# Optimization experiments

Measured on AMD Instinct MI355X. Metric: run time of the kernel, lower is better.

Reference implementation:

```python
import jax, jax.numpy as jnp
import numpy as np
import math

D_MODEL, NHEAD, N_LAYERS = 128, 8, 4
LAYER_NAMES = ("self", "cross", "self", "cross")
B, H, W = 2, 128, 160
MID = D_MODEL
D_FF = 2 * D_MODEL
BN_EPS = 1e-5
LN_EPS = 1e-5
ATTN_EPS = 1e-6


def setup_inputs() -> dict:
    key = jax.random.key(0)
    ks = iter(jax.random.split(key, 64))

    def rn(shape, scale):
        return jax.random.normal(next(ks), shape, dtype=jnp.float32) * scale

    inp = {}
    inp["ref_feature"] = rn((B, D_MODEL, H, W), 1.0)
    inp["src_feature"] = rn((B, D_MODEL, H, W), 1.0)
    K = np.array([[200.0, 0.0, W / 2.0], [0.0, 200.0, H / 2.0], [0.0, 0.0, 1.0]], np.float32)

    def make_proj(tx):
        E = np.eye(4, dtype=np.float32); E[0, 3] = tx
        P = np.eye(4, dtype=np.float32); P[:3, :4] = K @ E[:3, :4]
        return np.broadcast_to(P, (B, 4, 4)).astype(np.float32).copy()

    rp, sp = make_proj(0.0), make_proj(10.0)
    inp["ref_proj"] = jnp.asarray(rp)
    inp["src_proj"] = jnp.asarray(sp)
    inp["ref_img2world"] = jnp.asarray(np.linalg.inv(rp))
    inp["src_img2world"] = jnp.asarray(np.linalg.inv(sp))
    inp["depth_hypo"] = 500.0 + 100.0 * jax.random.uniform(next(ks), (B, 1, H, W), dtype=jnp.float32)
    xav = 0.08  # ~xavier std for 128x128
    inp["attn_w"] = rn((N_LAYERS, 4, D_MODEL, D_MODEL), xav)  # q,k,v,out
    inp["attn_b"] = jnp.zeros((N_LAYERS, 4, D_MODEL), jnp.float32)
    inp["ffn_w1"] = rn((N_LAYERS, D_MODEL, D_FF), 0.07)
    inp["ffn_b1"] = jnp.zeros((N_LAYERS, D_FF), jnp.float32)
    inp["ffn_w2"] = rn((N_LAYERS, D_FF, D_MODEL), 0.07)
    inp["ffn_b2"] = jnp.zeros((N_LAYERS, D_MODEL), jnp.float32)
    inp["ln_g"] = jnp.ones((N_LAYERS, 2, D_MODEL), jnp.float32)
    inp["ln_b"] = jnp.zeros((N_LAYERS, 2, D_MODEL), jnp.float32)
    inp["rc_w"] = rn((MID, 1, 3, 3), 0.01)
    inp["rc_b"] = jnp.zeros((MID,), jnp.float32)
    inp["bn2_g"] = jnp.ones((MID,), jnp.float32)
    inp["bn2_b"] = jnp.zeros((MID,), jnp.float32)
    inp["cc_w"] = rn((MID, D_MODEL), xav)
    inp["cc_b"] = jnp.zeros((D_MODEL,), jnp.float32)
    inp["bn1_g"] = jnp.ones((16,), jnp.float32)
    inp["bn1_b"] = jnp.zeros((16,), jnp.float32)
    inp["fc1_w"] = rn((16, MID), 0.16)
    inp["fc1_b"] = jnp.zeros((MID,), jnp.float32)
    inp["fc2_w"] = rn((MID, MID), xav)
    inp["fc2_b"] = jnp.zeros((MID,), jnp.float32)
    inp["ser_w"] = rn((MID, MID), xav)
    inp["ser_b"] = jnp.zeros((MID,), jnp.float32)
    inp["see_w"] = rn((MID, MID), xav)
    inp["see_b"] = jnp.zeros((MID,), jnp.float32)
    return inp


def sine_pe(d_model, Hh, Ww):
    # PositionEncodingSine (temp_bug_fix=True), computed only on the [H,W] slice
    y_pos = jnp.arange(1, Hh + 1, dtype=jnp.float32)[:, None] * jnp.ones((1, Ww), jnp.float32)
    x_pos = jnp.ones((Hh, 1), jnp.float32) * jnp.arange(1, Ww + 1, dtype=jnp.float32)[None, :]
    div = jnp.exp(jnp.arange(0, d_model // 2, 2, dtype=jnp.float32) * (-math.log(10000.0) / (d_model // 2)))[:, None, None]
    pe = jnp.stack([jnp.sin(x_pos * div), jnp.cos(x_pos * div), jnp.sin(y_pos * div), jnp.cos(y_pos * div)], axis=1)
    return pe.reshape(d_model, Hh, Ww)


def grid_sample_bilinear(feat, grid):
    # feat [B,C,Hs,Ws], grid [B,P,2] normalized to [-1,1]; align_corners=True, zeros padding
    Bn, C, Hs, Ws = feat.shape
    P = grid.shape[1]
    x = (grid[..., 0] + 1.0) * 0.5 * (Ws - 1)
    y = (grid[..., 1] + 1.0) * 0.5 * (Hs - 1)
    x0, y0 = jnp.floor(x), jnp.floor(y)
    wx, wy = x - x0, y - y0
    flat = feat.reshape(Bn, C, Hs * Ws)

    def gather(xi, yi):
        valid = (xi >= 0) & (xi <= Ws - 1) & (yi >= 0) & (yi <= Hs - 1)
        xi_c = jnp.clip(xi, 0, Ws - 1).astype(jnp.int32)
        yi_c = jnp.clip(yi, 0, Hs - 1).astype(jnp.int32)
        idx = yi_c * Ws + xi_c  # [B,P]
        v = jnp.take_along_axis(flat, jnp.broadcast_to(idx[:, None, :], (Bn, C, P)), axis=2)
        return v * valid[:, None, :].astype(feat.dtype)

    v00 = gather(x0, y0)
    v01 = gather(x0 + 1, y0)
    v10 = gather(x0, y0 + 1)
    v11 = gather(x0 + 1, y0 + 1)
    wx, wy = wx[:, None, :], wy[:, None, :]
    return v00 * (1 - wx) * (1 - wy) + v01 * wx * (1 - wy) + v10 * (1 - wx) * wy + v11 * wx * wy


def homo_warp_ref_to_src(feat, ref_proj, src_proj, depth):
    # homo_warping_pe with fea='ref': proj = ref_proj @ inv(src_proj)
    Bn, C, Hs, Ws = feat.shape
    _, D, Hr, Wr = depth.shape
    proj = jnp.einsum('bij,bjk->bik', ref_proj, jnp.linalg.inv(src_proj))
    rot, trans = proj[:, :3, :3], proj[:, :3, 3]
    yy, xx = jnp.meshgrid(jnp.arange(Hr, dtype=jnp.float32), jnp.arange(Wr, dtype=jnp.float32), indexing='ij')
    xyz = jnp.stack([xx.ravel(), yy.ravel(), jnp.ones(Hr * Wr, jnp.float32)], 0)  # [3, P]
    rot_xyz = jnp.einsum('bij,jp->bip', rot, xyz)  # [B,3,P]
    pxyz = rot_xyz[:, :, None, :] * depth.reshape(Bn, 1, D, Hr * Wr) + trans[:, :, None, None]
    z = pxyz[:, 2]
    z = jnp.where(z == 0, 1e-9, z)
    gx = (pxyz[:, 0] / z) / ((Ws - 1) / 2.0) - 1.0
    gy = (pxyz[:, 1] / z) / ((Hs - 1) / 2.0) - 1.0
    grid = jax.lax.stop_gradient(jnp.stack([gx, gy], -1).reshape(Bn, D * Hr * Wr, 2))  # torch no_grad
    out = grid_sample_bilinear(feat, grid)
    return out.reshape(Bn, C, D, Hr, Wr)


def layer_norm(x, g, b):
    mu = x.mean(-1, keepdims=True)
    var = ((x - mu) ** 2).mean(-1, keepdims=True)
    return (x - mu) * jax.lax.rsqrt(var + LN_EPS) * g + b


def encoder_layer(x, src, w, bb, w1, b1f, w2, b2f, g, bt):
    N, L, d = x.shape
    h, dh = NHEAD, d // NHEAD
    q = (x @ w[0] + bb[0]).reshape(N, L, h, dh)
    k = (src @ w[1] + bb[1]).reshape(N, -1, h, dh)
    v = (src @ w[2] + bb[2]).reshape(N, -1, h, dh)
    Q = jax.nn.elu(q) + 1.0
    K = jax.nn.elu(k) + 1.0
    KV = jnp.einsum('nshd,nshm->nhmd', K, v)
    Z = 1.0 / (jnp.einsum('nlhd,nhd->nlh', Q, K.sum(1)) + ATTN_EPS)
    V = jnp.einsum('nlhd,nhmd,nlh->nlhm', Q, KV, Z).reshape(N, L, d)
    x = x + (V @ w[3] + bb[3])
    x = layer_norm(x, g[0], bt[0])
    y = jax.nn.relu(x @ w1 + b1f) @ w2 + b2f
    return layer_norm(x + y, g[1], bt[1])


def cam_encode(feat, cam16, rc_w, rc_b, bn2_g, bn2_b, cc_w, cc_b, bn1_g, bn1_b,
               fc1_w, fc1_b, fc2_w, fc2_b, ser_w, ser_b, see_w, see_b):
    inv_std = 1.0 / jnp.sqrt(1.0 + BN_EPS)  # eval-mode BN, running stats (0,1)
    mlp_in = cam16 * inv_std * bn1_g + bn1_b
    hmap = jax.lax.conv_general_dilated(feat, rc_w, (1, 1), 'SAME', dimension_numbers=('NCHW', 'OIHW', 'NCHW')) + rc_b[None, :, None, None]
    hmap = jax.nn.relu(hmap * inv_std * bn2_g[None, :, None, None] + bn2_b[None, :, None, None])
    se = jax.nn.relu(mlp_in @ fc1_w + fc1_b) @ fc2_w + fc2_b  # [B, MID]
    gate = jax.nn.sigmoid(jax.nn.relu(se @ ser_w + ser_b) @ see_w + see_b)
    ctx = hmap * gate[:, :, None, None]
    return jnp.einsum('bchw,co->bohw', ctx, cc_w) + cc_b[None, :, None, None]


def reference(ref_feature, src_feature, ref_img2world, src_img2world, ref_proj, src_proj, depth_hypo,
              attn_w, attn_b, ffn_w1, ffn_b1, ffn_w2, ffn_b2, ln_g, ln_b,
              rc_w, rc_b, bn2_g, bn2_b, cc_w, cc_b, bn1_g, bn1_b,
              fc1_w, fc1_b, fc2_w, fc2_b, ser_w, ser_b, see_w, see_b):
    Bn, C, Hh, Ww = ref_feature.shape
    pe = sine_pe(C, Hh, Ww)[None]
    ref_ctx = cam_encode(depth_hypo, ref_img2world.reshape(Bn, 16), rc_w, rc_b, bn2_g, bn2_b,
                         cc_w, cc_b, bn1_g, bn1_b, fc1_w, fc1_b, fc2_w, fc2_b,
                         ser_w, ser_b, see_w, see_b)
    src_ctx = homo_warp_ref_to_src(ref_ctx, ref_proj, src_proj, depth_hypo)[:, :, 0]
    ref = (ref_feature + pe + ref_ctx).reshape(Bn, C, Hh * Ww).transpose(0, 2, 1)
    src = (src_feature + pe + src_ctx).reshape(Bn, C, Hh * Ww).transpose(0, 2, 1)
    for i, name in enumerate(LAYER_NAMES):
        p = (attn_w[i], attn_b[i], ffn_w1[i], ffn_b1[i], ffn_w2[i], ffn_b2[i], ln_g[i], ln_b[i])
        if name == 'self':
            ref = encoder_layer(ref, ref, *p)
            src = encoder_layer(src, src, *p)
        else:
            ref = encoder_layer(ref, src, *p)
            src = encoder_layer(src, ref, *p)
    return jnp.stack([ref, src])  # [2, B, H*W, C]
```

## Files before the change

kernel.cpp:

```cpp
#include <hip/hip_runtime.h>
#include <math.h>

#define BN 2
#define HH 128
#define WW 160
#define HWn (HH*WW)
#define CD 128
#define TT (BN*HWn)
#define TOKN ((size_t)TT*CD)

typedef __attribute__((ext_vector_type(8))) short bf16x8;
typedef __attribute__((ext_vector_type(4))) float f32x4;
typedef __attribute__((ext_vector_type(4))) unsigned short u16x4;

__device__ __forceinline__ float b2f(unsigned short s){
  unsigned u = ((unsigned)s) << 16;
  return __builtin_bit_cast(float, u);
}
__device__ __forceinline__ unsigned short f2b(float f){
  unsigned u = __builtin_bit_cast(unsigned, f);
  u = (u + 0x7fffu + ((u >> 16) & 1u)) >> 16;
  return (unsigned short)u;
}

__global__ void k_small(const float* __restrict__ ref_proj, const float* __restrict__ src_i2w,
                        const float* __restrict__ cam16,
                        const float* __restrict__ bn1_g, const float* __restrict__ bn1_b,
                        const float* __restrict__ fc1_w, const float* __restrict__ fc1_b,
                        const float* __restrict__ fc2_w, const float* __restrict__ fc2_b,
                        const float* __restrict__ ser_w, const float* __restrict__ ser_b,
                        const float* __restrict__ see_w, const float* __restrict__ see_b,
                        float* __restrict__ projsmall, float* __restrict__ gate){
  __shared__ float mi[BN][16], t1[BN][128], t2[BN][128];
  int tid = threadIdx.x;
  const float inv_std = rsqrtf(1.0f + 1e-5f);
  if (tid < 32){
    int b = tid >> 4, idx = tid & 15, i = idx >> 2, k = idx & 3;
    float acc = 0.f;
    for (int j = 0; j < 4; j++) acc += ref_proj[b*16 + i*4 + j] * src_i2w[b*16 + j*4 + k];
    if (i < 3 && k < 3) projsmall[b*12 + i*3 + k] = acc;
    if (i < 3 && k == 3) projsmall[b*12 + 9 + i] = acc;
    mi[b][idx] = cam16[b*16 + idx] * inv_std * bn1_g[idx] + bn1_b[idx];
  }
  __syncthreads();
  int b = tid >> 7, c = tid & 127;
  float a = 0.f;
  for (int j = 0; j < 16; j++) a += mi[b][j] * fc1_w[j*128 + c];
  t1[b][c] = fmaxf(a + fc1_b[c], 0.f);
  __syncthreads();
  a = 0.f;
  for (int k = 0; k < 128; k++) a += t1[b][k] * fc2_w[k*128 + c];
  t2[b][c] = a + fc2_b[c];
  __syncthreads();
  a = 0.f;
  for (int k = 0; k < 128; k++) a += t2[b][k] * ser_w[k*128 + c];
  t1[b][c] = fmaxf(a + ser_b[c], 0.f);
  __syncthreads();
  a = 0.f;
  for (int k = 0; k < 128; k++) a += t1[b][k] * see_w[k*128 + c];
  a += see_b[c];
  gate[b*128 + c] = 1.f / (1.f + __expf(-a));
}

__global__ __launch_bounds__(256) void k_wconv(const float* __restrict__ attn_w,
      const float* __restrict__ ffn_w1, const float* __restrict__ ffn_w2,
      const float* __restrict__ cc_w, unsigned short* __restrict__ wt){
  int i = blockIdx.x*256 + threadIdx.x;
  float v;
  if (i < 262144){
    int k = i & 127, n = (i >> 7) & 127, lm = i >> 14;
    v = attn_w[((size_t)lm*128 + k)*128 + n];
  } else if (i < 393216){ int j = i - 262144;
    int k = j & 127, n = (j >> 7) & 255, l = j >> 15;
    v = ffn_w1[((size_t)l*128 + k)*256 + n];
  } else if (i < 524288){ int j = i - 393216;
    int k = j & 255, n = (j >> 8) & 127, l = j >> 15;
    v = ffn_w2[((size_t)l*256 + k)*128 + n];
  } else if (i < 540672){ int j = i - 524288;
    int k = j & 127, n = j >> 7;
    v = cc_w[(size_t)k*128 + n];
  } else return;
  wt[i] = f2b(v);
}

__global__ __launch_bounds__(128) void k_hmap(const float* __restrict__ depth,
                       const float* __restrict__ rc_w, const float* __restrict__ rc_b,
                       const float* __restrict__ bn2_g, const float* __restrict__ bn2_b,
                       const float* __restrict__ gate, unsigned short* __restrict__ G){
  int bi = blockIdx.x; int n = bi / HWn; int p = bi - n*HWn;
  int y = p / WW, x = p - y*WW;
  int c = threadIdx.x;
  const float inv_std = rsqrtf(1.f + 1e-5f);
  float acc = 0.f;
#pragma unroll
  for (int ky = 0; ky < 3; ky++){
    int yy = y + ky - 1;
#pragma unroll
    for (int kx = 0; kx < 3; kx++){
      int xx = x + kx - 1;
      float v = (yy >= 0 && yy < HH && xx >= 0 && xx < WW) ? depth[n*HWn + yy*WW + xx] : 0.f;
      acc += v * rc_w[c*9 + ky*3 + kx];
    }
  }
  acc += rc_b[c];
  acc = fmaxf(acc * inv_std * bn2_g[c] + bn2_b[c], 0.f);
  G[(size_t)bi*128 + c] = f2b(acc * gate[n*128 + c]);
}

template<int K, int ACT, int LN>
__global__ __launch_bounds__(256) void k_bgemm6(
    const unsigned short* __restrict__ A, const unsigned short* __restrict__ A2, int ldA,
    const unsigned short* __restrict__ Wt,
    const float* __restrict__ bias, int amask,
    const unsigned short* __restrict__ resid,
    unsigned short* __restrict__ Cbase, size_t secStride, int ldC,
    const float* __restrict__ lng, const float* __restrict__ lnb){
  __shared__ unsigned short Wl[128*128];
  constexpr int NH = K/128;
  int tid = threadIdx.x;
  int wid = tid >> 6, lane = tid & 63;
  int sec = blockIdx.y;
  const unsigned short* Ab = (sec == 0) ? A : A2;
  const unsigned short* Ws = Wt + (size_t)sec*128*K;
  const float* bs = bias + sec*128;
  unsigned short* C = Cbase + (size_t)sec*secStride;
  int r = lane & 15, ks = lane >> 4;
  size_t t0 = (size_t)blockIdx.x*64 + wid*16;
  const unsigned short* ap = Ab + (t0 + r)*ldA + ks*8;
  f32x4 acc[8] = {};
#pragma unroll
  for (int hh = 0; hh < NH; hh++){
    if (hh > 0) __syncthreads();
#pragma unroll
    for (int i = 0; i < 8; i++){
      int idx = i*256 + tid;
      int row = idx >> 4, c8 = idx & 15;
      int c8s = c8 ^ (row & 7);
      *(bf16x8*)&Wl[row*128 + c8s*8] = *(const bf16x8*)(Ws + (size_t)row*K + hh*128 + c8*8);
    }
    __syncthreads();
#pragma unroll
    for (int j = 0; j < 4; j++){
      bf16x8 a = *(const bf16x8*)(ap + hh*128 + j*32);
#pragma unroll
      for (int f = 0; f < 8; f++){
        int row = f*16 + r;
        int c8s = (j*4 + ks) ^ (row & 7);
        bf16x8 w = *(const bf16x8*)&Wl[row*128 + c8s*8];
        acc[f] = __builtin_amdgcn_mfma_f32_16x16x32_bf16(w, a, acc[f], 0, 0, 0);
      }
    }
  }
  bool act = (amask >> sec) & 1;
  size_t trow = t0 + r;
  float vv[8][4];
#pragma unroll
  for (int f = 0; f < 8; f++){
    float4 bi4 = *(const float4*)&bs[f*16 + 4*ks];
    vv[f][0] = acc[f][0] + bi4.x; vv[f][1] = acc[f][1] + bi4.y;
    vv[f][2] = acc[f][2] + bi4.z; vv[f][3] = acc[f][3] + bi4.w;
    if (resid){
      u16x4 rr = *(const u16x4*)(resid + trow*128 + f*16 + 4*ks);
#pragma unroll
      for (int e = 0; e < 4; e++) vv[f][e] += b2f(rr[e]);
    }
    if (act){
#pragma unroll
      for (int e = 0; e < 4; e++){
        float x = vv[f][e];
        if (ACT == 1) x = fmaxf(x, 0.f);
        if (ACT == 2) x = x > 0.f ? x + 1.f : __expf(x);
        vv[f][e] = x;
      }
    }
  }
  if (LN){
    float s = 0.f;
#pragma unroll
    for (int f = 0; f < 8; f++) s += vv[f][0]+vv[f][1]+vv[f][2]+vv[f][3];
    s += __shfl_xor(s, 16, 64); s += __shfl_xor(s, 32, 64);
    float mean = s * (1.f/128.f);
    float q = 0.f;
#pragma unroll
    for (int f = 0; f < 8; f++)
#pragma unroll
      for (int e = 0; e < 4; e++){ float d = vv[f][e]-mean; q += d*d; }
    q += __shfl_xor(q, 16, 64); q += __shfl_xor(q, 32, 64);
    float rstd = rsqrtf(q*(1.f/128.f) + 1e-5f);
#pragma unroll
    for (int f = 0; f < 8; f++){
      float4 g4 = *(const float4*)&lng[f*16 + 4*ks];
      float4 b4 = *(const float4*)&lnb[f*16 + 4*ks];
      vv[f][0] = (vv[f][0]-mean)*rstd*g4.x + b4.x;
      vv[f][1] = (vv[f][1]-mean)*rstd*g4.y + b4.y;
      vv[f][2] = (vv[f][2]-mean)*rstd*g4.z + b4.z;
      vv[f][3] = (vv[f][3]-mean)*rstd*g4.w + b4.w;
    }
  }
#pragma unroll
  for (int f = 0; f < 8; f++){
    u16x4 o;
#pragma unroll
    for (int e = 0; e < 4; e++) o[e] = f2b(vv[f][e]);
    *(u16x4*)(C + trow*ldC + f*16 + 4*ks) = o;
  }
}

__global__ __launch_bounds__(256) void k_fffn(
    const unsigned short* __restrict__ A,
    const unsigned short* __restrict__ W1t, const float* __restrict__ b1,
    const unsigned short* __restrict__ W2t, const float* __restrict__ b2,
    const float* __restrict__ g1, const float* __restrict__ lb1,
    unsigned short* __restrict__ Out){
  __shared__ unsigned short Wl[128*128];
  __shared__ unsigned short Hs[64*256];
  int tid = threadIdx.x;
  int wid = tid >> 6, lane = tid & 63;
  int r = lane & 15, ks = lane >> 4;
  int tl = wid*16 + r;
  size_t trow = (size_t)blockIdx.x*64 + tl;
  const unsigned short* ap = A + trow*128 + ks*8;
  bf16x8 areg[4];
#pragma unroll
  for (int j = 0; j < 4; j++) areg[j] = *(const bf16x8*)(ap + j*32);
  int swl = tl & 7;
#pragma unroll
  for (int hh = 0; hh < 2; hh++){
    if (hh > 0) __syncthreads();
#pragma unroll
    for (int i = 0; i < 8; i++){
      int idx = i*256 + tid;
      int row = idx >> 4, c8 = idx & 15;
      *(bf16x8*)&Wl[row*128 + (c8 ^ (row & 7))*8] =
          *(const bf16x8*)(W1t + (size_t)(hh*128 + row)*128 + c8*8);
    }
    __syncthreads();
    f32x4 acc[8] = {};
#pragma unroll
    for (int j = 0; j < 4; j++){
#pragma unroll
      for (int f = 0; f < 8; f++){
        int row = f*16 + r;
        int c8s = (j*4 + ks) ^ (row & 7);
        bf16x8 w = *(const bf16x8*)&Wl[row*128 + c8s*8];
        acc[f] = __builtin_amdgcn_mfma_f32_16x16x32_bf16(w, areg[j], acc[f], 0, 0, 0);
      }
    }
#pragma unroll
    for (int f = 0; f < 8; f++){
      float4 bi4 = *(const float4*)&b1[hh*128 + f*16 + 4*ks];
      u16x4 o;
      o[0] = f2b(fmaxf(acc[f][0] + bi4.x, 0.f));
      o[1] = f2b(fmaxf(acc[f][1] + bi4.y, 0.f));
      o[2] = f2b(fmaxf(acc[f][2] + bi4.z, 0.f));
      o[3] = f2b(fmaxf(acc[f][3] + bi4.w, 0.f));
      int c8 = hh*16 + 2*f + (ks >> 1);
      *(u16x4*)&Hs[tl*256 + (c8 ^ swl)*8 + 4*(ks & 1)] = o;
    }
  }
  f32x4 acc2[8] = {};
#pragma unroll
  for (int hh = 0; hh < 2; hh++){
    __syncthreads();
#pragma unroll
    for (int i = 0; i < 8; i++){
      int idx = i*256 + tid;
      int row = idx >> 4, c8 = idx & 15;
      *(bf16x8*)&Wl[row*128 + (c8 ^ (row & 7))*8] =
          *(const bf16x8*)(W2t + (size_t)row*256 + hh*128 + c8*8);
    }
    __syncthreads();
#pragma unroll
    for (int j = 0; j < 4; j++){
      bf16x8 a = *(const bf16x8*)&Hs[tl*256 + ((hh*16 + j*4 + ks) ^ swl)*8];
#pragma unroll
      for (int f = 0; f < 8; f++){
        int row = f*16 + r;
        int c8s = (j*4 + ks) ^ (row & 7);
        bf16x8 w = *(const bf16x8*)&Wl[row*128 + c8s*8];
        acc2[f] = __builtin_amdgcn_mfma_f32_16x16x32_bf16(w, a, acc2[f], 0, 0, 0);
      }
    }
  }
  float vv[8][4];
#pragma unroll
  for (int f = 0; f < 8; f++){
    float4 bi4 = *(const float4*)&b2[f*16 + 4*ks];
    u16x4 rr = *(const u16x4*)(A + trow*128 + f*16 + 4*ks);
    vv[f][0] = acc2[f][0] + bi4.x + b2f(rr[0]);
    vv[f][1] = acc2[f][1] + bi4.y + b2f(rr[1]);
    vv[f][2] = acc2[f][2] + bi4.z + b2f(rr[2]);
    vv[f][3] = acc2[f][3] + bi4.w + b2f(rr[3]);
  }
  float s = 0.f;
#pragma unroll
  for (int f = 0; f < 8; f++) s += vv[f][0]+vv[f][1]+vv[f][2]+vv[f][3];
  s += __shfl_xor(s, 16, 64); s += __shfl_xor(s, 32, 64);
  float mean = s * (1.f/128.f);
  float q = 0.f;
#pragma unroll
  for (int f = 0; f < 8; f++)
#pragma unroll
    for (int e = 0; e < 4; e++){ float d = vv[f][e]-mean; q += d*d; }
  q += __shfl_xor(q, 16, 64); q += __shfl_xor(q, 32, 64);
  float rstd = rsqrtf(q*(1.f/128.f) + 1e-5f);
#pragma unroll
  for (int f = 0; f < 8; f++){
    float4 g4 = *(const float4*)&g1[f*16 + 4*ks];
    float4 b4 = *(const float4*)&lb1[f*16 + 4*ks];
    u16x4 o;
    o[0] = f2b((vv[f][0]-mean)*rstd*g4.x + b4.x);
    o[1] = f2b((vv[f][1]-mean)*rstd*g4.y + b4.y);
    o[2] = f2b((vv[f][2]-mean)*rstd*g4.z + b4.z);
    o[3] = f2b((vv[f][3]-mean)*rstd*g4.w + b4.w);
    *(u16x4*)(Out + trow*128 + f*16 + 4*ks) = o;
  }
}

__global__ __launch_bounds__(256) void k_fattn(
    const unsigned short* __restrict__ Q, const unsigned short* __restrict__ X,
    const float* __restrict__ kvfin, const unsigned short* __restrict__ W3,
    const float* __restrict__ b3, const float* __restrict__ g0, const float* __restrict__ b0,
    unsigned short* __restrict__ Out){
  __shared__ unsigned short Wl[128*128];
  __shared__ unsigned short QV[64][136];
  __shared__ float ksums[8][16];
  int tid = threadIdx.x;
  size_t tb = (size_t)blockIdx.x*64;
  int g = (int)(tb / HWn);
  const float* kvb = kvfin + g*2176;
  {
    int row = tid >> 1, half = tid & 1;
    int h = row >> 4, m = row & 15;
    int swz = row & 7;
#pragma unroll
    for (int c8i = 0; c8i < 8; c8i++){
      int c8 = half*8 + c8i;
      bf16x8 val = {};
      if ((c8 >> 1) == h){
        int d0 = (c8 & 1)*8;
        const float* src = kvb + h*272 + m*16 + d0;
#pragma unroll
        for (int e = 0; e < 8; e++) ((unsigned short*)&val)[e] = f2b(src[e]);
      }
      *(bf16x8*)&Wl[row*128 + (c8 ^ swz)*8] = val;
    }
  }
  if (tid < 128) ksums[tid >> 4][tid & 15] = kvb[(tid >> 4)*272 + 256 + (tid & 15)];
  __syncthreads();
  int wid = tid >> 6, lane = tid & 63;
  int r = lane & 15, ks = lane >> 4;
  int tl = wid*16 + r;
  size_t trow = tb + tl;
  f32x4 acc[8] = {};
  float part0 = 0.f, part1 = 0.f, part2 = 0.f, part3 = 0.f;
  int myp = ks >> 1;
  int dlo = (ks & 1)*8;
#pragma unroll
  for (int j = 0; j < 4; j++){
    bf16x8 a = *(const bf16x8*)(Q + trow*128 + j*32 + ks*8);
    float pj = 0.f;
    int hj = 2*j + myp;
#pragma unroll
    for (int e = 0; e < 8; e++)
      pj += b2f(((unsigned short*)&a)[e]) * ksums[hj][dlo + e];
    if (j == 0) part0 = pj; else if (j == 1) part1 = pj;
    else if (j == 2) part2 = pj; else part3 = pj;
#pragma unroll
    for (int f = 0; f < 8; f++){
      int row = f*16 + r;
      int c8s = (j*4 + ks) ^ (row & 7);
      bf16x8 w = *(const bf16x8*)&Wl[row*128 + c8s*8];
      acc[f] = __builtin_amdgcn_mfma_f32_16x16x32_bf16(w, a, acc[f], 0, 0, 0);
    }
  }
  float full0 = part0 + __shfl_xor(part0, 16, 64);
  float full1 = part1 + __shfl_xor(part1, 16, 64);
  float full2 = part2 + __shfl_xor(part2, 16, 64);
  float full3 = part3 + __shfl_xor(part3, 16, 64);
  float oth0 = __shfl_xor(full0, 32, 64);
  float oth1 = __shfl_xor(full1, 32, 64);
  float oth2 = __shfl_xor(full2, 32, 64);
  float oth3 = __shfl_xor(full3, 32, 64);
#pragma unroll
  for (int f = 0; f < 8; f++){
    float fl, ot;
    if (f < 2){ fl = full0; ot = oth0; } else if (f < 4){ fl = full1; ot = oth1; }
    else if (f < 6){ fl = full2; ot = oth2; } else { fl = full3; ot = oth3; }
    float den = ((f & 1) == myp) ? fl : ot;
    float rc = 1.f / (den + 1e-6f);
    u16x4 o;
#pragma unroll
    for (int e = 0; e < 4; e++) o[e] = f2b(acc[f][e] * rc);
    *(u16x4*)&QV[tl][f*16 + 4*ks] = o;
  }
  __syncthreads();
#pragma unroll
  for (int i = 0; i < 8; i++){
    int idx = i*256 + tid;
    int row = idx >> 4, c8 = idx & 15;
    int c8s = c8 ^ (row & 7);
    *(bf16x8*)&Wl[row*128 + c8s*8] = *(const bf16x8*)(W3 + (size_t)row*128 + c8*8);
  }
  __syncthreads();
  f32x4 acc2[8] = {};
#pragma unroll
  for (int j = 0; j < 4; j++){
    bf16x8 a = *(const bf16x8*)&QV[tl][j*32 + ks*8];
#pragma unroll
    for (int f = 0; f < 8; f++){
      int row = f*16 + r;
      int c8s = (j*4 + ks) ^ (row & 7);
      bf16x8 w = *(const bf16x8*)&Wl[row*128 + c8s*8];
      acc2[f] = __builtin_amdgcn_mfma_f32_16x16x32_bf16(w, a, acc2[f], 0, 0, 0);
    }
  }
  float vv[8][4];
#pragma unroll
  for (int f = 0; f < 8; f++){
    float4 bi4 = *(const float4*)&b3[f*16 + 4*ks];
    u16x4 rr = *(const u16x4*)(X + trow*128 + f*16 + 4*ks);
    vv[f][0] = acc2[f][0] + bi4.x + b2f(rr[0]);
    vv[f][1] = acc2[f][1] + bi4.y + b2f(rr[1]);
    vv[f][2] = acc2[f][2] + bi4.z + b2f(rr[2]);
    vv[f][3] = acc2[f][3] + bi4.w + b2f(rr[3]);
  }
  float s = 0.f;
#pragma unroll
  for (int f = 0; f < 8; f++) s += vv[f][0]+vv[f][1]+vv[f][2]+vv[f][3];
  s += __shfl_xor(s, 16, 64); s += __shfl_xor(s, 32, 64);
  float mean = s * (1.f/128.f);
  float q = 0.f;
#pragma unroll
  for (int f = 0; f < 8; f++)
#pragma unroll
    for (int e = 0; e < 4; e++){ float d = vv[f][e]-mean; q += d*d; }
  q += __shfl_xor(q, 16, 64); q += __shfl_xor(q, 32, 64);
  float rstd = rsqrtf(q*(1.f/128.f) + 1e-5f);
#pragma unroll
  for (int f = 0; f < 8; f++){
    float4 g4 = *(const float4*)&g0[f*16 + 4*ks];
    float4 b4 = *(const float4*)&b0[f*16 + 4*ks];
    u16x4 o;
    o[0] = f2b((vv[f][0]-mean)*rstd*g4.x + b4.x);
    o[1] = f2b((vv[f][1]-mean)*rstd*g4.y + b4.y);
    o[2] = f2b((vv[f][2]-mean)*rstd*g4.z + b4.z);
    o[3] = f2b((vv[f][3]-mean)*rstd*g4.w + b4.w);
    *(u16x4*)(Out + trow*128 + f*16 + 4*ks) = o;
  }
}

__global__ __launch_bounds__(256) void k_kvpart(const unsigned short* __restrict__ Kb,
                         const unsigned short* __restrict__ Vb, float* __restrict__ part){
  __shared__ float Ks[16][260], Vs[16][260];
  int bi = blockIdx.x;
  int chunk = bi % 80; int h = (bi / 80) & 7; int g = bi / 640;
  int s0 = chunk * 256;
  int tid = threadIdx.x;
#pragma unroll
  for (int rr = 0; rr < 8; rr++){
    int idx = rr*256 + tid;
    int s = idx >> 3, d2 = idx & 7;
    size_t gg = ((size_t)(g*HWn + s0 + s))*128 + h*16 + d2*2;
    Ks[d2*2  ][s] = b2f(Kb[gg]);
    Ks[d2*2+1][s] = b2f(Kb[gg+1]);
    Vs[d2*2  ][s] = b2f(Vb[gg]);
    Vs[d2*2+1][s] = b2f(Vb[gg+1]);
  }
  __syncthreads();
  int m = tid >> 4, d = tid & 15;
  float acc = 0.f, ksum = 0.f;
#pragma unroll 4
  for (int s4 = 0; s4 < 64; s4++){
    float4 kv = *(const float4*)&Ks[d][s4*4];
    float4 vv = *(const float4*)&Vs[m][s4*4];
    acc  += kv.x*vv.x + kv.y*vv.y + kv.z*vv.z + kv.w*vv.w;
    ksum += kv.x + kv.y + kv.z + kv.w;
  }
  part[(size_t)bi*272 + tid] = acc;
  if (m == 0) part[(size_t)bi*272 + 256 + d] = ksum;
}

__global__ void k_kvreduce(const float* __restrict__ part, float* __restrict__ fin){
  int nh = blockIdx.x;
  int o = threadIdx.x;
  if (o < 272){
    float acc = 0.f;
    for (int c2 = 0; c2 < 80; c2++) acc += part[((size_t)nh*80 + c2)*272 + o];
    fin[nh*272 + o] = acc;
  }
}

__global__ __launch_bounds__(128) void k_warp(const unsigned short* __restrict__ ctxref,
     const float* __restrict__ depth, const float* __restrict__ projs,
     unsigned short* __restrict__ ctxsrc){
  int bi = blockIdx.x; int n = bi / HWn; int p = bi - n*HWn;
  int y = p / WW, x = p - y*WW;
  const float* pr = &projs[n*12];
  float d = depth[n*HWn + p];
  float fx = (float)x, fy = (float)y;
  float px = (pr[0]*fx + pr[1]*fy + pr[2])*d + pr[9];
  float py = (pr[3]*fx + pr[4]*fy + pr[5])*d + pr[10];
  float pz = (pr[6]*fx + pr[7]*fy + pr[8])*d + pr[11];
  if (pz == 0.f) pz = 1e-9f;
  float xs = px/pz, ys = py/pz;
  float x0 = floorf(xs), y0 = floorf(ys);
  float wx = xs - x0, wy = ys - y0;
  int c = threadIdx.x;
  float acc = 0.f;
#pragma unroll
  for (int dy = 0; dy < 2; dy++){
    float cy = y0 + dy;
    float wyv = dy ? wy : 1.f - wy;
#pragma unroll
    for (int dx = 0; dx < 2; dx++){
      float cx = x0 + dx;
      float wxv = dx ? wx : 1.f - wx;
      bool valid = (cx >= 0.f) && (cx <= (float)(WW-1)) && (cy >= 0.f) && (cy <= (float)(HH-1));
      int xi = (int)fminf(fmaxf(cx, 0.f), (float)(WW-1));
      int yi = (int)fminf(fmaxf(cy, 0.f), (float)(HH-1));
      float v = b2f(ctxref[((size_t)(n*HWn) + yi*WW + xi)*128 + c]);
      acc += valid ? wxv*wyv*v : 0.f;
    }
  }
  ctxsrc[(size_t)bi*128 + c] = f2b(acc);
}

__global__ __launch_bounds__(256) void k_build(const float* __restrict__ feat,
      const unsigned short* __restrict__ ctx, unsigned short* __restrict__ out){
  __shared__ float tile[32][33];
  int tx = threadIdx.x, ty = threadIdx.y;
  int p0 = blockIdx.x*32, c0 = blockIdx.y*32, b = blockIdx.z;
  for (int i = ty; i < 32; i += 8)
    tile[i][tx] = feat[((size_t)(b*CD + c0 + i))*HWn + p0 + tx];
  __syncthreads();
  const float LOG1E4_32 = 0.28782313662425572f;
  for (int r = ty; r < 32; r += 8){
    int p = p0 + r, c = c0 + tx;
    int y = p / WW, x = p - y*WW;
    int i = c >> 2, j = c & 3;
    float dv = __expf(-(float)i * LOG1E4_32);
    float pos = (j < 2) ? (float)(x + 1) : (float)(y + 1);
    float arg = pos * dv;
    float pe = (j & 1) ? cosf(arg) : sinf(arg);
    size_t o = ((size_t)(b*HWn) + p)*128 + c;
    out[o] = f2b(tile[tx][r] + pe + b2f(ctx[o]));
  }
}

__global__ __launch_bounds__(256) void k_tofp32(const unsigned short* __restrict__ s,
                                                float* __restrict__ out){
  size_t i = ((size_t)blockIdx.x*256 + threadIdx.x)*4;
  u16x4 v = *(const u16x4*)(s + i);
  float4 o = { b2f(v[0]), b2f(v[1]), b2f(v[2]), b2f(v[3]) };
  *(float4*)(out + i) = o;
}

extern "C" void kernel_launch(void* const* d_in, const int* in_sizes, int n_in,
                              void* d_out, int out_size, void* d_ws, size_t ws_size,
                              hipStream_t stream) {
  const float* ref_feature = (const float*)d_in[0];
  const float* src_feature = (const float*)d_in[1];
  const float* ref_proj    = (const float*)d_in[2];
  const float* ref_i2w     = (const float*)d_in[4];
  const float* src_i2w     = (const float*)d_in[5];
  const float* depth       = (const float*)d_in[6];
  const float* attn_w      = (const float*)d_in[7];
  const float* attn_b      = (const float*)d_in[8];
  const float* ffn_w1      = (const float*)d_in[9];
  const float* ffn_b1      = (const float*)d_in[10];
  const float* ffn_w2      = (const float*)d_in[11];
  const float* ffn_b2      = (const float*)d_in[12];
  const float* ln_g        = (const float*)d_in[13];
  const float* ln_b        = (const float*)d_in[14];
  const float* rc_w        = (const float*)d_in[15];
  const float* rc_b        = (const float*)d_in[16];
  const float* bn2_g       = (const float*)d_in[17];
  const float* bn2_b       = (const float*)d_in[18];
  const float* cc_w        = (const float*)d_in[19];
  const float* cc_b        = (const float*)d_in[20];
  const float* bn1_g       = (const float*)d_in[21];
  const float* bn1_b       = (const float*)d_in[22];
  const float* fc1_w       = (const float*)d_in[23];
  const float* fc1_b       = (const float*)d_in[24];
  const float* fc2_w       = (const float*)d_in[25];
  const float* fc2_b       = (const float*)d_in[26];
  const float* ser_w       = (const float*)d_in[27];
  const float* ser_b       = (const float*)d_in[28];
  const float* see_w       = (const float*)d_in[29];
  const float* see_b       = (const float*)d_in[30];

  const size_t small_f32 = (size_t)4*640*272 + 4*2176 + 32 + 256;
  const size_t small_bytes = small_f32*4 + (size_t)540672*2 + 4096;
  const size_t need_batch = (size_t)TOKN*2*8 + small_bytes;
  bool BATCH = ws_size >= need_batch;
  const size_t CSEG = BATCH ? 2*TOKN : TOKN;

  char* p = (char*)d_ws;
  unsigned short* Rm = (unsigned short*)p; p += TOKN*2;
  unsigned short* Sm = (unsigned short*)p; p += TOKN*2;
  unsigned short* QB = (unsigned short*)p; p += CSEG*3*2;
  unsigned short* KB = QB + CSEG;
  unsigned short* VB = QB + 2*CSEG;
  float* KVPART = (float*)p; p += (size_t)(BATCH?4:2)*640*272*4;
  float* KVFIN  = (float*)p; p += (size_t)(BATCH?4:2)*2176*4;
  float* PROJ   = (float*)p; p += 32*4;
  float* GATE   = (float*)p; p += 256*4;
  unsigned short* WT = (unsigned short*)p;

  float* OUT = (float*)d_out;

  k_wconv<<<2112, 256, 0, stream>>>(attn_w, ffn_w1, ffn_w2, cc_w, WT);
  k_small<<<1, 256, 0, stream>>>(ref_proj, src_i2w, ref_i2w, bn1_g, bn1_b, fc1_w, fc1_b,
                                 fc2_w, fc2_b, ser_w, ser_b, see_w, see_b, PROJ, GATE);
  k_hmap<<<TT, 128, 0, stream>>>(depth, rc_w, rc_b, bn2_g, bn2_b, GATE, QB);
  k_bgemm6<128,0,0><<<dim3(TT/64, 1), 256, 0, stream>>>(
      QB, QB, 128, WT + 524288, cc_b, 0, nullptr, KB, 0, 128, nullptr, nullptr);
  k_warp<<<TT, 128, 0, stream>>>(KB, depth, PROJ, VB);
  k_build<<<dim3(HWn/32, 4, BN), dim3(32, 8), 0, stream>>>(ref_feature, KB, Rm);
  k_build<<<dim3(HWn/32, 4, BN), dim3(32, 8), 0, stream>>>(src_feature, VB, Sm);

  auto encode = [&](unsigned short* x, const unsigned short* srcp, int l, int nTok){
    const unsigned short* ATW = WT + (size_t)l*65536;
    const unsigned short* F1T = WT + 262144 + (size_t)l*32768;
    const unsigned short* F2T = WT + 393216 + (size_t)l*32768;
    const float* Bv = attn_b + (size_t)l*512;
    const float* g0 = ln_g + (size_t)l*256; const float* b0 = ln_b + (size_t)l*256;
    int nb = nTok/64, ng = nTok/HWn;
    k_bgemm6<128,2,0><<<dim3(nb, 3), 256, 0, stream>>>(x, srcp, 128, ATW, Bv, 0b011,
                                              nullptr, QB, CSEG, 128, nullptr, nullptr);
    k_kvpart<<<ng*640, 256, 0, stream>>>(KB, VB, KVPART);
    k_kvreduce<<<ng*8, 320, 0, stream>>>(KVPART, KVFIN);
    k_fattn<<<nb, 256, 0, stream>>>(QB, x, KVFIN, ATW + 3*16384, Bv + 384, g0, b0, QB);
    k_fffn<<<nb, 256, 0, stream>>>(QB, F1T, ffn_b1 + (size_t)l*256, F2T,
                                   ffn_b2 + (size_t)l*128, g0 + 128, b0 + 128, x);
  };

  if (BATCH) encode(Rm, Rm, 0, 2*TT);
  else { encode(Rm, Rm, 0, TT); encode(Sm, Sm, 0, TT); }
  encode(Rm, Sm, 1, TT); encode(Sm, Rm, 1, TT);
  if (BATCH) encode(Rm, Rm, 2, 2*TT);
  else { encode(Rm, Rm, 2, TT); encode(Sm, Sm, 2, TT); }
  encode(Rm, Sm, 3, TT); encode(Sm, Rm, 3, TT);

  k_tofp32<<<(unsigned)(2*TOKN/(256*4)), 256, 0, stream>>>(Rm, OUT);
}
```

Measured before the change: 625.0 us.

## Fuse attention output projection and FFN into a single kernel

Merges k_fattn (attention output, out-projection, residual, LayerNorm) and k_fffn (two-layer FFN, residual, LayerNorm) into one kernel, k_fattnffn. The post-LN activations stay in registers and shared memory instead of round-tripping through global memory, and one launch per encoder layer is removed. Shared memory is reused through a single union buffer. The trade-off is higher register pressure and extra syncs in one longer kernel, which may lower occupancy.

```diff
diff --git a/kernel.cpp b/kernel.cpp
--- a/kernel.cpp
+++ b/kernel.cpp
@@ -206,124 +206,16 @@
   }
 }
 
-__global__ __launch_bounds__(256) void k_fffn(
-    const unsigned short* __restrict__ A,
+__global__ __launch_bounds__(256) void k_fattnffn(
+    const unsigned short* __restrict__ Q, const unsigned short* __restrict__ X,
+    const float* __restrict__ kvfin, const unsigned short* __restrict__ W3,
+    const float* __restrict__ b3, const float* __restrict__ g0, const float* __restrict__ b0,
     const unsigned short* __restrict__ W1t, const float* __restrict__ b1,
     const unsigned short* __restrict__ W2t, const float* __restrict__ b2,
     const float* __restrict__ g1, const float* __restrict__ lb1,
     unsigned short* __restrict__ Out){
   __shared__ unsigned short Wl[128*128];
-  __shared__ unsigned short Hs[64*256];
-  int tid = threadIdx.x;
-  int wid = tid >> 6, lane = tid & 63;
-  int r = lane & 15, ks = lane >> 4;
-  int tl = wid*16 + r;
-  size_t trow = (size_t)blockIdx.x*64 + tl;
-  const unsigned short* ap = A + trow*128 + ks*8;
-  bf16x8 areg[4];
-#pragma unroll
-  for (int j = 0; j < 4; j++) areg[j] = *(const bf16x8*)(ap + j*32);
-  int swl = tl & 7;
-#pragma unroll
-  for (int hh = 0; hh < 2; hh++){
-    if (hh > 0) __syncthreads();
-#pragma unroll
-    for (int i = 0; i < 8; i++){
-      int idx = i*256 + tid;
-      int row = idx >> 4, c8 = idx & 15;
-      *(bf16x8*)&Wl[row*128 + (c8 ^ (row & 7))*8] =
-          *(const bf16x8*)(W1t + (size_t)(hh*128 + row)*128 + c8*8);
-    }
-    __syncthreads();
-    f32x4 acc[8] = {};
-#pragma unroll
-    for (int j = 0; j < 4; j++){
-#pragma unroll
-      for (int f = 0; f < 8; f++){
-        int row = f*16 + r;
-        int c8s = (j*4 + ks) ^ (row & 7);
-        bf16x8 w = *(const bf16x8*)&Wl[row*128 + c8s*8];
-        acc[f] = __builtin_amdgcn_mfma_f32_16x16x32_bf16(w, areg[j], acc[f], 0, 0, 0);
-      }
-    }
-#pragma unroll
-    for (int f = 0; f < 8; f++){
-      float4 bi4 = *(const float4*)&b1[hh*128 + f*16 + 4*ks];
-      u16x4 o;
-      o[0] = f2b(fmaxf(acc[f][0] + bi4.x, 0.f));
-      o[1] = f2b(fmaxf(acc[f][1] + bi4.y, 0.f));
-      o[2] = f2b(fmaxf(acc[f][2] + bi4.z, 0.f));
-      o[3] = f2b(fmaxf(acc[f][3] + bi4.w, 0.f));
-      int c8 = hh*16 + 2*f + (ks >> 1);
-      *(u16x4*)&Hs[tl*256 + (c8 ^ swl)*8 + 4*(ks & 1)] = o;
-    }
-  }
-  f32x4 acc2[8] = {};
-#pragma unroll
-  for (int hh = 0; hh < 2; hh++){
-    __syncthreads();
-#pragma unroll
-    for (int i = 0; i < 8; i++){
-      int idx = i*256 + tid;
-      int row = idx >> 4, c8 = idx & 15;
-      *(bf16x8*)&Wl[row*128 + (c8 ^ (row & 7))*8] =
-          *(const bf16x8*)(W2t + (size_t)row*256 + hh*128 + c8*8);
-    }
-    __syncthreads();
-#pragma unroll
-    for (int j = 0; j < 4; j++){
-      bf16x8 a = *(const bf16x8*)&Hs[tl*256 + ((hh*16 + j*4 + ks) ^ swl)*8];
-#pragma unroll
-      for (int f = 0; f < 8; f++){
-        int row = f*16 + r;
-        int c8s = (j*4 + ks) ^ (row & 7);
-        bf16x8 w = *(const bf16x8*)&Wl[row*128 + c8s*8];
-        acc2[f] = __builtin_amdgcn_mfma_f32_16x16x32_bf16(w, a, acc2[f], 0, 0, 0);
-      }
-    }
-  }
-  float vv[8][4];
-#pragma unroll
-  for (int f = 0; f < 8; f++){
-    float4 bi4 = *(const float4*)&b2[f*16 + 4*ks];
-    u16x4 rr = *(const u16x4*)(A + trow*128 + f*16 + 4*ks);
-    vv[f][0] = acc2[f][0] + bi4.x + b2f(rr[0]);
-    vv[f][1] = acc2[f][1] + bi4.y + b2f(rr[1]);
-    vv[f][2] = acc2[f][2] + bi4.z + b2f(rr[2]);
-    vv[f][3] = acc2[f][3] + bi4.w + b2f(rr[3]);
-  }
-  float s = 0.f;
-#pragma unroll
-  for (int f = 0; f < 8; f++) s += vv[f][0]+vv[f][1]+vv[f][2]+vv[f][3];
-  s += __shfl_xor(s, 16, 64); s += __shfl_xor(s, 32, 64);
-  float mean = s * (1.f/128.f);
-  float q = 0.f;
-#pragma unroll
-  for (int f = 0; f < 8; f++)
-#pragma unroll
-    for (int e = 0; e < 4; e++){ float d = vv[f][e]-mean; q += d*d; }
-  q += __shfl_xor(q, 16, 64); q += __shfl_xor(q, 32, 64);
-  float rstd = rsqrtf(q*(1.f/128.f) + 1e-5f);
-#pragma unroll
-  for (int f = 0; f < 8; f++){
-    float4 g4 = *(const float4*)&g1[f*16 + 4*ks];
-    float4 b4 = *(const float4*)&lb1[f*16 + 4*ks];
-    u16x4 o;
-    o[0] = f2b((vv[f][0]-mean)*rstd*g4.x + b4.x);
-    o[1] = f2b((vv[f][1]-mean)*rstd*g4.y + b4.y);
-    o[2] = f2b((vv[f][2]-mean)*rstd*g4.z + b4.z);
-    o[3] = f2b((vv[f][3]-mean)*rstd*g4.w + b4.w);
-    *(u16x4*)(Out + trow*128 + f*16 + 4*ks) = o;
-  }
-}
-
-__global__ __launch_bounds__(256) void k_fattn(
-    const unsigned short* __restrict__ Q, const unsigned short* __restrict__ X,
-    const float* __restrict__ kvfin, const unsigned short* __restrict__ W3,
-    const float* __restrict__ b3, const float* __restrict__ g0, const float* __restrict__ b0,
-    unsigned short* __restrict__ Out){
-  __shared__ unsigned short Wl[128*128];
-  __shared__ unsigned short QV[64][136];
+  __shared__ unsigned short UB[64*256];
   __shared__ float ksums[8][16];
   int tid = threadIdx.x;
   size_t tb = (size_t)blockIdx.x*64;
@@ -392,21 +284,20 @@
     u16x4 o;
 #pragma unroll
     for (int e = 0; e < 4; e++) o[e] = f2b(acc[f][e] * rc);
-    *(u16x4*)&QV[tl][f*16 + 4*ks] = o;
+    *(u16x4*)&UB[tl*136 + f*16 + 4*ks] = o;
   }
   __syncthreads();
 #pragma unroll
   for (int i = 0; i < 8; i++){
     int idx = i*256 + tid;
     int row = idx >> 4, c8 = idx & 15;
-    int c8s = c8 ^ (row & 7);
-    *(bf16x8*)&Wl[row*128 + c8s*8] = *(const bf16x8*)(W3 + (size_t)row*128 + c8*8);
+    *(bf16x8*)&Wl[row*128 + (c8 ^ (row & 7))*8] = *(const bf16x8*)(W3 + (size_t)row*128 + c8*8);
   }
   __syncthreads();
   f32x4 acc2[8] = {};
 #pragma unroll
   for (int j = 0; j < 4; j++){
-    bf16x8 a = *(const bf16x8*)&QV[tl][j*32 + ks*8];
+    bf16x8 a = *(const bf16x8*)&UB[tl*136 + j*32 + ks*8];
 #pragma unroll
     for (int f = 0; f < 8; f++){
       int row = f*16 + r;
@@ -425,6 +316,107 @@
     vv[f][2] = acc2[f][2] + bi4.z + b2f(rr[2]);
     vv[f][3] = acc2[f][3] + bi4.w + b2f(rr[3]);
   }
+  {
+    float s = 0.f;
+#pragma unroll
+    for (int f = 0; f < 8; f++) s += vv[f][0]+vv[f][1]+vv[f][2]+vv[f][3];
+    s += __shfl_xor(s, 16, 64); s += __shfl_xor(s, 32, 64);
+    float mean = s * (1.f/128.f);
+    float q = 0.f;
+#pragma unroll
+    for (int f = 0; f < 8; f++)
+#pragma unroll
+      for (int e = 0; e < 4; e++){ float d = vv[f][e]-mean; q += d*d; }
+    q += __shfl_xor(q, 16, 64); q += __shfl_xor(q, 32, 64);
+    float rstd = rsqrtf(q*(1.f/128.f) + 1e-5f);
+#pragma unroll
+    for (int f = 0; f < 8; f++){
+      float4 g4 = *(const float4*)&g0[f*16 + 4*ks];
+      float4 b4 = *(const float4*)&b0[f*16 + 4*ks];
+      vv[f][0] = (vv[f][0]-mean)*rstd*g4.x + b4.x;
+      vv[f][1] = (vv[f][1]-mean)*rstd*g4.y + b4.y;
+      vv[f][2] = (vv[f][2]-mean)*rstd*g4.z + b4.z;
+      vv[f][3] = (vv[f][3]-mean)*rstd*g4.w + b4.w;
+    }
+  }
+  u16x4 xr[8];
+#pragma unroll
+  for (int f = 0; f < 8; f++){
+#pragma unroll
+    for (int e = 0; e < 4; e++) xr[f][e] = f2b(vv[f][e]);
+    *(u16x4*)&UB[tl*136 + f*16 + 4*ks] = xr[f];
+  }
+  __syncthreads();
+  bf16x8 areg[4];
+#pragma unroll
+  for (int j = 0; j < 4; j++) areg[j] = *(const bf16x8*)&UB[tl*136 + j*32 + ks*8];
+  int swl = tl & 7;
+#pragma unroll
+  for (int hh = 0; hh < 2; hh++){
+#pragma unroll
+    for (int i = 0; i < 8; i++){
+      int idx = i*256 + tid;
+      int row = idx >> 4, c8 = idx & 15;
+      *(bf16x8*)&Wl[row*128 + (c8 ^ (row & 7))*8] =
+          *(const bf16x8*)(W1t + (size_t)(hh*128 + row)*128 + c8*8);
+    }
+    __syncthreads();
+    f32x4 accf[8] = {};
+#pragma unroll
+    for (int j = 0; j < 4; j++){
+#pragma unroll
+      for (int f = 0; f < 8; f++){
+        int row = f*16 + r;
+        int c8s = (j*4 + ks) ^ (row & 7);
+        bf16x8 w = *(const bf16x8*)&Wl[row*128 + c8s*8];
+        accf[f] = __builtin_amdgcn_mfma_f32_16x16x32_bf16(w, areg[j], accf[f], 0, 0, 0);
+      }
+    }
+#pragma unroll
+    for (int f = 0; f < 8; f++){
+      float4 bi4 = *(const float4*)&b1[hh*128 + f*16 + 4*ks];
+      u16x4 o;
+      o[0] = f2b(fmaxf(accf[f][0] + bi4.x, 0.f));
+      o[1] = f2b(fmaxf(accf[f][1] + bi4.y, 0.f));
+      o[2] = f2b(fmaxf(accf[f][2] + bi4.z, 0.f));
+      o[3] = f2b(fmaxf(accf[f][3] + bi4.w, 0.f));
+      int c8 = hh*16 + 2*f + (ks >> 1);
+      *(u16x4*)&UB[tl*256 + (c8 ^ swl)*8 + 4*(ks & 1)] = o;
+    }
+    __syncthreads();
+  }
+  f32x4 acc3[8] = {};
+#pragma unroll
+  for (int hh = 0; hh < 2; hh++){
+#pragma unroll
+    for (int i = 0; i < 8; i++){
+      int idx = i*256 + tid;
+      int row = idx >> 4, c8 = idx & 15;
+      *(bf16x8*)&Wl[row*128 + (c8 ^ (row & 7))*8] =
+          *(const bf16x8*)(W2t + (size_t)row*256 + hh*128 + c8*8);
+    }
+    __syncthreads();
+#pragma unroll
+    for (int j = 0; j < 4; j++){
+      bf16x8 a = *(const bf16x8*)&UB[tl*256 + ((hh*16 + j*4 + ks) ^ swl)*8];
+#pragma unroll
+      for (int f = 0; f < 8; f++){
+        int row = f*16 + r;
+        int c8s = (j*4 + ks) ^ (row & 7);
+        bf16x8 w = *(const bf16x8*)&Wl[row*128 + c8s*8];
+        acc3[f] = __builtin_amdgcn_mfma_f32_16x16x32_bf16(w, a, acc3[f], 0, 0, 0);
+      }
+    }
+    if (hh == 0) __syncthreads();
+  }
+#pragma unroll
+  for (int f = 0; f < 8; f++){
+    float4 bi4 = *(const float4*)&b2[f*16 + 4*ks];
+    vv[f][0] = acc3[f][0] + bi4.x + b2f(xr[f][0]);
+    vv[f][1] = acc3[f][1] + bi4.y + b2f(xr[f][1]);
+    vv[f][2] = acc3[f][2] + bi4.z + b2f(xr[f][2]);
+    vv[f][3] = acc3[f][3] + bi4.w + b2f(xr[f][3]);
+  }
   float s = 0.f;
 #pragma unroll
   for (int f = 0; f < 8; f++) s += vv[f][0]+vv[f][1]+vv[f][2]+vv[f][3];
@@ -439,8 +431,8 @@
   float rstd = rsqrtf(q*(1.f/128.f) + 1e-5f);
 #pragma unroll
   for (int f = 0; f < 8; f++){
-    float4 g4 = *(const float4*)&g0[f*16 + 4*ks];
-    float4 b4 = *(const float4*)&b0[f*16 + 4*ks];
+    float4 g4 = *(const float4*)&g1[f*16 + 4*ks];
+    float4 b4 = *(const float4*)&lb1[f*16 + 4*ks];
     u16x4 o;
     o[0] = f2b((vv[f][0]-mean)*rstd*g4.x + b4.x);
     o[1] = f2b((vv[f][1]-mean)*rstd*g4.y + b4.y);
@@ -631,9 +623,9 @@
                                               nullptr, QB, CSEG, 128, nullptr, nullptr);
     k_kvpart<<<ng*640, 256, 0, stream>>>(KB, VB, KVPART);
     k_kvreduce<<<ng*8, 320, 0, stream>>>(KVPART, KVFIN);
-    k_fattn<<<nb, 256, 0, stream>>>(QB, x, KVFIN, ATW + 3*16384, Bv + 384, g0, b0, QB);
-    k_fffn<<<nb, 256, 0, stream>>>(QB, F1T, ffn_b1 + (size_t)l*256, F2T,
-                                   ffn_b2 + (size_t)l*128, g0 + 128, b0 + 128, x);
+    k_fattnffn<<<nb, 256, 0, stream>>>(QB, x, KVFIN, ATW + 3*16384, Bv + 384, g0, b0,
+                                       F1T, ffn_b1 + (size_t)l*256, F2T,
+                                       ffn_b2 + (size_t)l*128, g0 + 128, b0 + 128, x);
   };
 
   if (BATCH) encode(Rm, Rm, 0, 2*TT);
```

Measured after the change: 589.3 us. 5.7% less time.
